# Kernel optimization log

Measured on AMD Instinct MI355X. Metric: run time of the kernel, lower is better.

Reference implementation:

```python
import jax, jax.numpy as jnp
import numpy as np

DIM = 768
H = 12
HEAD = DIM // H
SCALE = HEAD ** -0.5
NMM, NV, NA = 8, 4, 4


def _cross_attn(x1, x2, qw, kvw, pw, pb):
    # x1: [B,N1,C] queries, x2: [B,N2,C] keys/values. Weights stored [in,out].
    B, N1, C = x1.shape
    N2 = x2.shape[1]
    q = (x1 @ qw).reshape(B, N1, H, HEAD).transpose(0, 2, 1, 3)        # [B,H,N1,d]
    kv = (x2 @ kvw).reshape(B, N2, 2, H, HEAD)
    k = kv[:, :, 0].transpose(0, 2, 1, 3)                               # [B,H,N2,d]
    v = kv[:, :, 1].transpose(0, 2, 1, 3)
    attn = jax.nn.softmax(jnp.einsum('bhnd,bhmd->bhnm', q, k) * SCALE, axis=-1)
    o = jnp.einsum('bhnm,bhmd->bhnd', attn, v).transpose(0, 2, 1, 3).reshape(B, N1, C)
    return o @ pw + pb, attn


def setup_inputs() -> dict:
    key = jax.random.key(0)
    ks = jax.random.split(key, 16)
    s = 0.02
    inp = {
        'xmm': jax.random.normal(ks[0], (64, 16, DIM), jnp.float32),
        'xv': jax.random.normal(ks[1], (64, 784, DIM), jnp.float32),
        'xa': jax.random.normal(ks[2], (64, 512, DIM), jnp.float32),
        # visual cross-attn params (weights stored [in,out] = torch W.T)
        'qv_w': s * jax.random.normal(ks[3], (DIM, DIM), jnp.float32),
        'kvv_w': s * jax.random.normal(ks[4], (DIM, 2 * DIM), jnp.float32),
        'projv_w': s * jax.random.normal(ks[5], (DIM, DIM), jnp.float32),
        'projv_b': jnp.zeros((DIM,), jnp.float32),
        # audio cross-attn params
        'qa_w': s * jax.random.normal(ks[6], (DIM, DIM), jnp.float32),
        'kva_w': s * jax.random.normal(ks[7], (DIM, 2 * DIM), jnp.float32),
        'proja_w': s * jax.random.normal(ks[8], (DIM, DIM), jnp.float32),
        'proja_b': jnp.zeros((DIM,), jnp.float32),
        # factorized fusion attention params (dim_ratio=1.0 -> inner dim = DIM)
        'fq_w': s * jax.random.normal(ks[9], (DIM, DIM), jnp.float32),
        'fk_w': s * jax.random.normal(ks[10], (2 * DIM, DIM), jnp.float32),
        'fv_w': s * jax.random.normal(ks[11], (2 * DIM, DIM), jnp.float32),
        'fproj_w': s * jax.random.normal(ks[12], (DIM, DIM), jnp.float32),
        'fproj_b': jnp.zeros((DIM,), jnp.float32),
    }
    return inp


def reference(xmm, xv, xa, qv_w, kvv_w, projv_w, projv_b,
              qa_w, kva_w, proja_w, proja_b,
              fq_w, fk_w, fv_w, fproj_w, fproj_b):
    B = xmm.shape[0]
    xmm2 = xmm[:, :NMM]
    xmm_v, _ = _cross_attn(xmm[:, NMM:NMM + NV], xv, qv_w, kvv_w, projv_w, projv_b)
    xmm_a, _ = _cross_attn(xmm[:, NMM + NV:], xa, qa_w, kva_w, proja_w, proja_b)
    # outer-product token fusion: [B, NV*NA, 2*DIM]
    xva = jnp.concatenate([
        jnp.broadcast_to(xmm_v[:, :, None, :], (B, NV, NA, DIM)),
        jnp.broadcast_to(xmm_a[:, None, :, :], (B, NV, NA, DIM)),
    ], axis=-1).reshape(B, NV * NA, 2 * DIM)
    q = (xmm2 @ fq_w).reshape(B, NMM, H, -1).transpose(0, 2, 1, 3)
    k = (xva @ fk_w).reshape(B, NV * NA, H, -1).transpose(0, 2, 1, 3)
    v = (xva @ fv_w).reshape(B, NV * NA, H, -1).transpose(0, 2, 1, 3)
    attn = jax.nn.softmax(jnp.einsum('bhnd,bhmd->bhnm', q, k) * SCALE, axis=-1)
    o = jnp.einsum('bhnm,bhmd->bhnd', attn, v).transpose(0, 2, 1, 3).reshape(B, NMM, DIM)
    o = o @ fproj_w + fproj_b
    xmm_out = jnp.concatenate([o, xmm_v, xmm_a], axis=1)  # [B,16,DIM]
    return xmm_out, attn
```

## Files before the change

### kernel.cpp

```cpp
#include <hip/hip_runtime.h>
#include <stdint.h>

typedef unsigned short u16;
typedef unsigned int u32;
typedef __attribute__((ext_vector_type(8))) short short8;
typedef __attribute__((ext_vector_type(4))) float floatx4;


__device__ __forceinline__ u16 f2bf_rne(float f) {
  u32 u = __float_as_uint(f);
  return (u16)((u + 0x7fffu + ((u >> 16) & 1u)) >> 16);
}
__device__ __forceinline__ u32 pack_rne_u(u32 a, u32 b) {
  a += 0x7fffu + ((a >> 16) & 1u);
  b += 0x7fffu + ((b >> 16) & 1u);
  return __builtin_amdgcn_perm(b, a, 0x07060302u);
}

__device__ __forceinline__ void block_sync_lds() {
  asm volatile("s_waitcnt lgkmcnt(0)" ::: "memory");
  __builtin_amdgcn_s_barrier();
  asm volatile("" ::: "memory");
}

__device__ __forceinline__ void sg_body(
    float (*sAt)[20], float (*sW)[64],
    const float* __restrict__ A, int a_pitch, int a_rb, int a_off,
    const float* __restrict__ W, const float* __restrict__ bias,
    float* __restrict__ Cout, int c_pitch, int c_rb, int c_off,
    int rt, int n0)
{
  const int t = threadIdx.x;
  const int g = t >> 6;
  const int c = t & 63;

  float acc[4] = {0.f, 0.f, 0.f, 0.f};

  for (int ks = 0; ks < 12; ++ks) {
    {
      int r = t >> 4;
      int c4 = (t & 15) * 4;
      int lr = rt * 16 + r;
      int grow = (lr / a_rb) * a_pitch + a_off + (lr % a_rb);
      float4 v = *(const float4*)(A + (size_t)grow * 768 + ks * 64 + c4);
      sAt[c4 + 0][r] = v.x;
      sAt[c4 + 1][r] = v.y;
      sAt[c4 + 2][r] = v.z;
      sAt[c4 + 3][r] = v.w;
    }
#pragma unroll
    for (int u = 0; u < 4; ++u) {
      int unit = t + u * 256;
      int r = unit >> 4;
      int c4 = (unit & 15) * 4;
      *(float4*)&sW[r][c4] = *(const float4*)(W + (size_t)(ks * 64 + r) * 768 + n0 + c4);
    }
    __syncthreads();
#pragma unroll 8
    for (int k = 0; k < 64; ++k) {
      float4 a4 = *(const float4*)&sAt[k][g * 4];
      float w = sW[k][c];
      acc[0] += a4.x * w;
      acc[1] += a4.y * w;
      acc[2] += a4.z * w;
      acc[3] += a4.w * w;
    }
    __syncthreads();
  }

  float bs = bias ? bias[n0 + c] : 0.f;
#pragma unroll
  for (int rr = 0; rr < 4; ++rr) {
    int lr = rt * 16 + g * 4 + rr;
    int grow = (lr / c_rb) * c_pitch + c_off + (lr % c_rb);
    Cout[(size_t)grow * 768 + n0 + c] = acc[rr] + bs;
  }
}

__global__ __launch_bounds__(256) void qproj(
    const float* __restrict__ xmm,
    const float* __restrict__ qv_w, const float* __restrict__ qa_w,
    const float* __restrict__ fq_w,
    float* __restrict__ q_v, float* __restrict__ q_a, float* __restrict__ q_f)
{
  __shared__ float sAt[64][20];
  __shared__ float sW[64][64];
  int rt = blockIdx.x;
  int n0 = blockIdx.y * 64;
  if (rt < 16)
    sg_body(sAt, sW, xmm, 16, 4, 8, qv_w, nullptr, q_v, 4, 4, 0, rt, n0);
  else if (rt < 32)
    sg_body(sAt, sW, xmm, 16, 4, 12, qa_w, nullptr, q_a, 4, 4, 0, rt - 16, n0);
  else
    sg_body(sAt, sW, xmm, 16, 8, 0, fq_w, nullptr, q_f, 8, 8, 0, rt - 32, n0);
}

__global__ __launch_bounds__(256) void proj2(
    const float* __restrict__ o_v, const float* __restrict__ o_a,
    const float* __restrict__ projv_w, const float* __restrict__ projv_b,
    const float* __restrict__ proja_w, const float* __restrict__ proja_b,
    float* __restrict__ out0)
{
  __shared__ float sAt[64][20];
  __shared__ float sW[64][64];
  int z = blockIdx.z;
  sg_body(sAt, sW, z ? o_a : o_v, 4, 4, 0,
          z ? proja_w : projv_w, z ? proja_b : projv_b,
          out0, 16, 4, z ? 12 : 8, blockIdx.x, blockIdx.y * 64);
}

__global__ __launch_bounds__(256) void fkv(
    const float* __restrict__ out0,
    const float* __restrict__ fk_w, const float* __restrict__ fv_w,
    float* __restrict__ kbase)
{
  __shared__ float sAt[64][20];
  __shared__ float sW[64][64];
  int z = blockIdx.z;
  const float* W = (z < 2) ? (fk_w + (size_t)(z & 1) * 768 * 768)
                           : (fv_w + (size_t)(z & 1) * 768 * 768);
  int a_off = (z & 1) ? 12 : 8;
  sg_body(sAt, sW, out0, 16, 4, a_off, W, nullptr,
          kbase + (size_t)z * 256 * 768, 4, 4, 0, blockIdx.x, blockIdx.y * 64);
}

__global__ __launch_bounds__(256) void fproj(
    const float* __restrict__ o_f,
    const float* __restrict__ fproj_w, const float* __restrict__ fproj_b,
    float* __restrict__ out0)
{
  __shared__ float sAt[64][20];
  __shared__ float sW[64][64];
  sg_body(sAt, sW, o_f, 8, 8, 0, fproj_w, fproj_b, out0, 16, 8, 0,
          blockIdx.x, blockIdx.y * 64);
}

__global__ __launch_bounds__(256) void qtilde(
    const float* __restrict__ q_v, const float* __restrict__ q_a,
    const float* __restrict__ kvv_w, const float* __restrict__ kva_w,
    u16* __restrict__ Qt_v, u16* __restrict__ Qt_a)
{
  __shared__ float sAt[64][20];
  __shared__ float sW[64][65];

  const int rt = blockIdx.x;
  const int nt = blockIdx.y;
  const int path = blockIdx.z / 12;
  const int h = blockIdx.z % 12;
  const float* q = path ? q_a : q_v;
  const float* kvw = path ? kva_w : kvv_w;
  u16* Qt = path ? Qt_a : Qt_v;

  const int t = threadIdx.x;
  const int g = t >> 6;
  const int c = t & 63;
  const int n0 = nt * 64;

  {
    int r = t >> 4;
    int c4 = (t & 15) * 4;
    float4 v = *(const float4*)(q + (size_t)(rt * 16 + r) * 768 + h * 64 + c4);
    sAt[c4 + 0][r] = v.x;
    sAt[c4 + 1][r] = v.y;
    sAt[c4 + 2][r] = v.z;
    sAt[c4 + 3][r] = v.w;
  }
#pragma unroll
  for (int u = 0; u < 4; ++u) {
    int unit = t + u * 256;
    int d = unit >> 4;
    int c4 = (unit & 15) * 4;
    float4 v = *(const float4*)(kvw + (size_t)(n0 + d) * 1536 + h * 64 + c4);
    sW[d][c4 + 0] = v.x;
    sW[d][c4 + 1] = v.y;
    sW[d][c4 + 2] = v.z;
    sW[d][c4 + 3] = v.w;
  }
  __syncthreads();

  float acc[4] = {0.f, 0.f, 0.f, 0.f};
#pragma unroll 16
  for (int e = 0; e < 64; ++e) {
    float4 a4 = *(const float4*)&sAt[e][g * 4];
    float w = sW[c][e];
    acc[0] += a4.x * w;
    acc[1] += a4.y * w;
    acc[2] += a4.z * w;
    acc[3] += a4.w * w;
  }
#pragma unroll
  for (int rr = 0; rr < 4; ++rr) {
    int rl = rt * 16 + g * 4 + rr;
    Qt[((size_t)(rl >> 2) * 48 + h * 4 + (rl & 3)) * 768 + n0 + c] = f2bf_rne(acc[rr]);
  }
}

__global__ __launch_bounds__(256) void attn_logits(
    const u16* __restrict__ Qt_v, const u16* __restrict__ Qt_a,
    const float* __restrict__ Xv, const float* __restrict__ Xa,
    float* __restrict__ Sv, float* __restrict__ Sa)
{
  const int z = blockIdx.z;
  const int jt = blockIdx.x;
  if (z == 1 && jt >= 4) return;
  const u16* Qt = z ? Qt_a : Qt_v;
  const float* X = z ? Xa : Xv;
  float* S = z ? Sa : Sv;
  const int N2 = z ? 512 : 784;

  __shared__ __align__(16) u16 sX[2][128 * 64];

  const int t = threadIdx.x;
  const int lane = t & 63;
  const int wave = t >> 6;
  const int b = blockIdx.y;
  const int j0 = jt * 128;
  const int jmax = (N2 - j0 < 128) ? (N2 - j0) : 128;
  const u16* Qb = Qt + (size_t)b * 48 * 768;
  const float* Xb = X + (size_t)b * N2 * 768;

  const int xr_r = t >> 3;
  const int xc = (t & 7) * 8;
  const int qrow0 = lane & 15;
  const int qcb = (lane >> 4) * 8;

  floatx4 acc[3][2];
#pragma unroll
  for (int i = 0; i < 3; ++i)
#pragma unroll
    for (int j = 0; j < 2; ++j) acc[i][j] = (floatx4){0.f, 0.f, 0.f, 0.f};

  uint4 xA[4][2], xB[4][2];
  short8 qr[3][2];

#define AL_LOADX(dst, ks_)                                                     \
  do {                                                                         \
    _Pragma("unroll") for (int u = 0; u < 4; ++u) {                            \
      int r_ = xr_r + u * 32;                                                  \
      uint4 a0_ = {0u, 0u, 0u, 0u}, a1_ = {0u, 0u, 0u, 0u};                    \
      if (r_ < jmax) {                                                         \
        const uint4* s_ =                                                      \
            (const uint4*)(Xb + (size_t)(j0 + r_) * 768 + (ks_) * 64 + xc);    \
        a0_ = s_[0];                                                           \
        a1_ = s_[1];                                                           \
      }                                                                        \
      dst[u][0] = a0_;                                                         \
      dst[u][1] = a1_;                                                         \
    }                                                                          \
  } while (0)

#define AL_LOADQ(ks_)                                                          \
  do {                                                                         \
    _Pragma("unroll") for (int i = 0; i < 3; ++i)                              \
      _Pragma("unroll") for (int kk = 0; kk < 2; ++kk)                         \
        qr[i][kk] = *(const short8*)(Qb + (size_t)(i * 16 + qrow0) * 768 +     \
                                     (ks_) * 64 + kk * 32 + qcb);              \
  } while (0)

#define AL_WRITEX(src, bufp)                                                   \
  do {                                                                         \
    _Pragma("unroll") for (int u = 0; u < 4; ++u) {                            \
      int r_ = xr_r + u * 32;                                                  \
      uint4 pk_;                                                               \
      pk_.x = pack_rne_u(src[u][0].x, src[u][0].y);                            \
      pk_.y = pack_rne_u(src[u][0].z, src[u][0].w);                            \
      pk_.z = pack_rne_u(src[u][1].x, src[u][1].y);                            \
      pk_.w = pack_rne_u(src[u][1].z, src[u][1].w);                            \
      *(uint4*)((bufp) + r_ * 64 + (xc ^ ((r_ & 7) * 8))) = pk_;               \
    }                                                                          \
  } while (0)

#define AL_COMPUTE(bufp)                                                       \
  do {                                                                         \
    _Pragma("unroll") for (int kk = 0; kk < 2; ++kk) {                         \
      short8 bfr_[2];                                                          \
      _Pragma("unroll") for (int jj = 0; jj < 2; ++jj) {                       \
        int jr_ = wave * 32 + jj * 16 + qrow0;                                 \
        int kb_ = kk * 32 + qcb;                                               \
        bfr_[jj] =                                                             \
            *(const short8*)((bufp) + jr_ * 64 + (kb_ ^ ((jr_ & 7) * 8)));     \
      }                                                                        \
      _Pragma("unroll") for (int i = 0; i < 3; ++i)                            \
        _Pragma("unroll") for (int jj = 0; jj < 2; ++jj)                       \
          acc[i][jj] = __builtin_amdgcn_mfma_f32_16x16x32_bf16(                \
              qr[i][kk], bfr_[jj], acc[i][jj], 0, 0, 0);                       \
    }                                                                          \
  } while (0)

  u16* sX0 = &sX[0][0];
  u16* sX1 = &sX[1][0];

  AL_LOADX(xA, 0);
  AL_LOADQ(0);
#pragma unroll
  for (int ks = 0; ks < 12; ks += 2) {
    AL_LOADX(xB, ks + 1);
    AL_WRITEX(xA, sX0);
    block_sync_lds();
    AL_COMPUTE(sX0);
    AL_LOADQ(ks + 1);
    if (ks + 2 < 12) AL_LOADX(xA, ks + 2);
    AL_WRITEX(xB, sX1);
    block_sync_lds();
    AL_COMPUTE(sX1);
    if (ks + 2 < 12) AL_LOADQ(ks + 2);
  }
#undef AL_LOADX
#undef AL_LOADQ
#undef AL_WRITEX
#undef AL_COMPUTE

  const int quad = lane >> 4;
  const int lc = lane & 15;
#pragma unroll
  for (int i = 0; i < 3; ++i)
#pragma unroll
    for (int jj = 0; jj < 2; ++jj) {
      int col = j0 + wave * 32 + jj * 16 + lc;
      if (col < N2) {
        int row0 = i * 16 + quad * 4;
#pragma unroll
        for (int r = 0; r < 4; ++r)
          S[((size_t)b * 48 + row0 + r) * N2 + col] = acc[i][jj][r] * 0.125f;
      }
    }
}

__global__ __launch_bounds__(256) void softmax_p(
    const float* __restrict__ Sv, const float* __restrict__ Sa,
    u16* __restrict__ Pv, u16* __restrict__ Pa)
{
  const int z = blockIdx.z;
  const float* S = z ? Sa : Sv;
  u16* P = z ? Pa : Pv;
  const int N2 = z ? 512 : 784;
  const int N2p = z ? 512 : 832;

  const int hh = blockIdx.x;
  const int b = blockIdx.y;
  const int t = threadIdx.x;
  const int lane = t & 63;
  const int wave = t >> 6;
  const int row = hh * 4 + wave;
  const float* Srow = S + ((size_t)b * 48 + row) * N2;
  u16* Prow = P + ((size_t)b * 48 + row) * N2p;

  float m = -1e30f;
  for (int j = lane; j < N2; j += 64) m = fmaxf(m, Srow[j]);
#pragma unroll
  for (int off = 32; off > 0; off >>= 1) m = fmaxf(m, __shfl_xor(m, off));

  float e[13];
  float l = 0.f;
  int cnt = 0;
  for (int j = lane; j < N2; j += 64) {
    float p = __expf(Srow[j] - m);
    e[cnt++] = p;
    l += p;
  }
#pragma unroll
  for (int off = 32; off > 0; off >>= 1) l += __shfl_xor(l, off);
  float inv = 1.0f / l;

  cnt = 0;
  for (int j = lane; j < N2; j += 64) Prow[j] = f2bf_rne(e[cnt++] * inv);
  for (int j = N2 + lane; j < N2p; j += 64) Prow[j] = 0;
}

__global__ __launch_bounds__(256) void attn_px(
    const u16* __restrict__ Pv, const u16* __restrict__ Pa,
    const float* __restrict__ Xv, const float* __restrict__ Xa,
    float* __restrict__ Ov, float* __restrict__ Oa)
{
  const int z = blockIdx.z;
  const u16* P = z ? Pa : Pv;
  const float* X = z ? Xa : Xv;
  float* O = z ? Oa : Ov;
  const int N2 = z ? 512 : 784;
  const int N2p = z ? 512 : 832;

  __shared__ __align__(16) u16 sXT[2][128 * 72];

  const int t = threadIdx.x;
  const int lane = t & 63;
  const int wave = t >> 6;
  const int nt = blockIdx.x;
  const int b = blockIdx.y;
  const int n0 = nt * 128;
  const u16* Pb = P + (size_t)b * 48 * N2p;
  const float* Xb = X + (size_t)b * N2 * 768;
  const int Ks = N2p >> 6;

  const int jp0 = t >> 5;
  const int nq4 = (t & 31) * 4;
  const int qrow0 = lane & 15;
  const int qcb = (lane >> 4) * 8;

  floatx4 acc[3][2];
#pragma unroll
  for (int i = 0; i < 3; ++i)
#pragma unroll
    for (int j = 0; j < 2; ++j) acc[i][j] = (floatx4){0.f, 0.f, 0.f, 0.f};

  uint4 xA[4][2], xB[4][2];
  short8 qr[3][2];

#define PX_LOADX(dst, ks_)                                                     \
  do {                                                                         \
    _Pragma("unroll") for (int u = 0; u < 4; ++u) {                            \
      int j_ = (ks_) * 64 + (jp0 + u * 8) * 2;                                 \
      uint4 a0_ = {0u, 0u, 0u, 0u}, a1_ = {0u, 0u, 0u, 0u};                    \
      if (j_ < N2)                                                             \
        a0_ = *(const uint4*)(Xb + (size_t)j_ * 768 + n0 + nq4);               \
      if (j_ + 1 < N2)                                                         \
        a1_ = *(const uint4*)(Xb + (size_t)(j_ + 1) * 768 + n0 + nq4);         \
      dst[u][0] = a0_;                                                         \
      dst[u][1] = a1_;                                                         \
    }                                                                          \
  } while (0)

#define PX_LOADP(ks_)                                                          \
  do {                                                                         \
    _Pragma("unroll") for (int i = 0; i < 3; ++i)                              \
      _Pragma("unroll") for (int kk = 0; kk < 2; ++kk)                         \
        qr[i][kk] = *(const short8*)(Pb + (size_t)(i * 16 + qrow0) * N2p +     \
                                     (ks_) * 64 + kk * 32 + qcb);              \
  } while (0)

#define PX_WRITEX(src, bufp)                                                   \
  do {                                                                         \
    _Pragma("unroll") for (int u = 0; u < 4; ++u) {                            \
      int jl_ = (jp0 + u * 8) * 2;                                             \
      u32 w0_ = pack_rne_u(src[u][0].x, src[u][1].x);                          \
      u32 w1_ = pack_rne_u(src[u][0].y, src[u][1].y);                          \
      u32 w2_ = pack_rne_u(src[u][0].z, src[u][1].z);                          \
      u32 w3_ = pack_rne_u(src[u][0].w, src[u][1].w);                          \
      _Pragma("unroll") for (int m_ = 0; m_ < 4; ++m_) {                       \
        int n_ = nq4 + m_;                                                     \
        int sw_ = (((n_ >> 2) & 7) ^ ((n_ & 3) << 1)) * 8;                     \
        u32 wv_ = (m_ == 0) ? w0_ : (m_ == 1) ? w1_ : (m_ == 2) ? w2_ : w3_;   \
        *(u32*)((bufp) + n_ * 72 + (jl_ ^ sw_)) = wv_;                         \
      }                                                                        \
    }                                                                          \
  } while (0)

#define PX_COMPUTE(bufp)                                                       \
  do {                                                                         \
    _Pragma("unroll") for (int kk = 0; kk < 2; ++kk) {                         \
      _Pragma("unroll") for (int jj = 0; jj < 2; ++jj) {                       \
        int n_ = wave * 32 + jj * 16 + qrow0;                                  \
        int sw_ = (((n_ >> 2) & 7) ^ ((n_ & 3) << 1)) * 8;                     \
        int kb_ = kk * 32 + qcb;                                               \
        short8 bfr_ = *(const short8*)((bufp) + n_ * 72 + (kb_ ^ sw_));        \
        _Pragma("unroll") for (int i = 0; i < 3; ++i)                          \
          acc[i][jj] = __builtin_amdgcn_mfma_f32_16x16x32_bf16(                \
              qr[i][kk], bfr_, acc[i][jj], 0, 0, 0);                           \
      }                                                                        \
    }                                                                          \
  } while (0)

  u16* sT0 = &sXT[0][0];
  u16* sT1 = &sXT[1][0];

  PX_LOADX(xA, 0);
  PX_LOADP(0);
  int ks = 0;
  for (;;) {
    int more0 = (ks + 1 < Ks);
    if (more0) PX_LOADX(xB, ks + 1);
    PX_WRITEX(xA, sT0);
    block_sync_lds();
    PX_COMPUTE(sT0);
    if (!more0) break;
    PX_LOADP(ks + 1);
    ++ks;
    int more1 = (ks + 1 < Ks);
    if (more1) PX_LOADX(xA, ks + 1);
    PX_WRITEX(xB, sT1);
    block_sync_lds();
    PX_COMPUTE(sT1);
    if (!more1) break;
    PX_LOADP(ks + 1);
    ++ks;
  }
#undef PX_LOADX
#undef PX_LOADP
#undef PX_WRITEX
#undef PX_COMPUTE

  const int quad = lane >> 4;
  const int lc = lane & 15;
#pragma unroll
  for (int i = 0; i < 3; ++i)
#pragma unroll
    for (int jj = 0; jj < 2; ++jj) {
      int col = n0 + wave * 32 + jj * 16 + lc;
      int row0 = i * 16 + quad * 4;
#pragma unroll
      for (int r = 0; r < 4; ++r)
        O[((size_t)b * 48 + row0 + r) * 768 + col] = acc[i][jj][r];
    }
}

__global__ __launch_bounds__(256) void omix(
    const float* __restrict__ O_v, const float* __restrict__ O_a,
    const float* __restrict__ kvv_w, const float* __restrict__ kva_w,
    float* __restrict__ o_v, float* __restrict__ o_a)
{
  __shared__ float sAt[64][20];
  __shared__ float sW[64][64];

  const int z = blockIdx.z;
  const float* Ob = z ? O_a : O_v;
  const float* kvw = z ? kva_w : kvv_w;
  float* oo = z ? o_a : o_v;

  const int rt = blockIdx.x;
  const int h = blockIdx.y;
  const int t = threadIdx.x;
  const int g = t >> 6;
  const int c = t & 63;

  float acc[4] = {0.f, 0.f, 0.f, 0.f};

  for (int ks = 0; ks < 12; ++ks) {
    {
      int r = t >> 4;
      int c4 = (t & 15) * 4;
      int rl = rt * 16 + r;
      int arow = (rl >> 2) * 48 + h * 4 + (rl & 3);
      float4 v = *(const float4*)(Ob + (size_t)arow * 768 + ks * 64 + c4);
      sAt[c4 + 0][r] = v.x;
      sAt[c4 + 1][r] = v.y;
      sAt[c4 + 2][r] = v.z;
      sAt[c4 + 3][r] = v.w;
    }
#pragma unroll
    for (int u = 0; u < 4; ++u) {
      int unit = t + u * 256;
      int k = unit >> 4;
      int c4 = (unit & 15) * 4;
      *(float4*)&sW[k][c4] = *(const float4*)(kvw + (size_t)(ks * 64 + k) * 1536 + 768 + h * 64 + c4);
    }
    __syncthreads();
#pragma unroll 8
    for (int k = 0; k < 64; ++k) {
      float4 a4 = *(const float4*)&sAt[k][g * 4];
      float w = sW[k][c];
      acc[0] += a4.x * w;
      acc[1] += a4.y * w;
      acc[2] += a4.z * w;
      acc[3] += a4.w * w;
    }
    __syncthreads();
  }

#pragma unroll
  for (int rr = 0; rr < 4; ++rr) {
    int rl = rt * 16 + g * 4 + rr;
    oo[(size_t)rl * 768 + h * 64 + c] = acc[rr];
  }
}

__global__ __launch_bounds__(256) void fusion_attn(
    const float* __restrict__ Qf,
    const float* __restrict__ K1, const float* __restrict__ K2,
    const float* __restrict__ V1, const float* __restrict__ V2,
    float* __restrict__ Of,
    float* __restrict__ AttnOut)
{
  const int h = blockIdx.x;
  const int b = blockIdx.y;
  const int t = threadIdx.x;
  const int lane = t & 63;
  const int wave = t >> 6;

  __shared__ float sQ[8][64];
  __shared__ float sK1[4][64], sK2[4][64], sV1[4][64], sV2[4][64];
  __shared__ float sP[8][16];

  for (int idx = t; idx < 512; idx += 256)
    sQ[idx >> 6][idx & 63] = Qf[((size_t)(b * 8 + (idx >> 6))) * 768 + h * 64 + (idx & 63)];
  {
    size_t base = ((size_t)(b * 4 + wave)) * 768 + h * 64 + lane;
    sK1[wave][lane] = K1[base];
    sK2[wave][lane] = K2[base];
    sV1[wave][lane] = V1[base];
    sV2[wave][lane] = V2[base];
  }
  __syncthreads();

  if (t < 128) {
    int qi = t >> 4, m = t & 15, iv = m >> 2, ja = m & 3;
    float s = 0.f;
#pragma unroll
    for (int d = 0; d < 64; ++d) s += sQ[qi][d] * (sK1[iv][d] + sK2[ja][d]);
    s *= 0.125f;
    float mx = s;
#pragma unroll
    for (int off = 8; off > 0; off >>= 1) mx = fmaxf(mx, __shfl_xor(mx, off, 16));
    float p = __expf(s - mx);
    float l = p;
#pragma unroll
    for (int off = 8; off > 0; off >>= 1) l += __shfl_xor(l, off, 16);
    p = p / l;
    sP[qi][m] = p;
    AttnOut[(((size_t)b * 12 + h) * 8 + qi) * 16 + m] = p;
  }
  __syncthreads();

  for (int idx = t; idx < 512; idx += 256) {
    int qi = idx >> 6, d = idx & 63;
    float o = 0.f;
#pragma unroll
    for (int m = 0; m < 16; ++m) o += sP[qi][m] * (sV1[m >> 2][d] + sV2[m & 3][d]);
    Of[((size_t)(b * 8 + qi)) * 768 + h * 64 + d] = o;
  }
}

extern "C" void kernel_launch(void* const* d_in, const int* in_sizes, int n_in,
                              void* d_out, int out_size, void* d_ws, size_t ws_size,
                              hipStream_t stream)
{
  const float* xmm     = (const float*)d_in[0];
  const float* xv      = (const float*)d_in[1];
  const float* xa      = (const float*)d_in[2];
  const float* qv_w    = (const float*)d_in[3];
  const float* kvv_w   = (const float*)d_in[4];
  const float* projv_w = (const float*)d_in[5];
  const float* projv_b = (const float*)d_in[6];
  const float* qa_w    = (const float*)d_in[7];
  const float* kva_w   = (const float*)d_in[8];
  const float* proja_w = (const float*)d_in[9];
  const float* proja_b = (const float*)d_in[10];
  const float* fq_w    = (const float*)d_in[11];
  const float* fk_w    = (const float*)d_in[12];
  const float* fv_w    = (const float*)d_in[13];
  const float* fproj_w = (const float*)d_in[14];
  const float* fproj_b = (const float*)d_in[15];

  float* out0 = (float*)d_out;
  float* out1 = out0 + (size_t)64 * 16 * 768;

  char* ws = (char*)d_ws;
  size_t off = 0;
  float* q_v  = (float*)(ws + off); off += (size_t)256 * 768 * 4;
  float* q_a  = (float*)(ws + off); off += (size_t)256 * 768 * 4;
  float* q_f  = (float*)(ws + off); off += (size_t)512 * 768 * 4;
  u16*   Qt_v = (u16*)(ws + off);   off += (size_t)64 * 48 * 768 * 2;
  u16*   Qt_a = (u16*)(ws + off);   off += (size_t)64 * 48 * 768 * 2;
  float* S_v  = (float*)(ws + off); off += (size_t)64 * 48 * 784 * 4;
  float* S_a  = (float*)(ws + off); off += (size_t)64 * 48 * 512 * 4;
  u16*   P_v  = (u16*)(ws + off);   off += (size_t)64 * 48 * 832 * 2;
  u16*   P_a  = (u16*)(ws + off);   off += (size_t)64 * 48 * 512 * 2;
  float* O_v  = (float*)(ws + off); off += (size_t)64 * 48 * 768 * 4;
  float* O_a  = (float*)(ws + off); off += (size_t)64 * 48 * 768 * 4;
  float* o_v  = (float*)(ws + off); off += (size_t)256 * 768 * 4;
  float* o_a  = (float*)(ws + off); off += (size_t)256 * 768 * 4;
  float* kbase = (float*)(ws + off); off += (size_t)4 * 256 * 768 * 4;
  float* o_f  = (float*)(ws + off); off += (size_t)512 * 768 * 4;

  float* k1 = kbase;
  float* k2 = kbase + (size_t)256 * 768;
  float* v1 = kbase + (size_t)2 * 256 * 768;
  float* v2 = kbase + (size_t)3 * 256 * 768;

  qproj<<<dim3(64, 12), 256, 0, stream>>>(xmm, qv_w, qa_w, fq_w, q_v, q_a, q_f);
  qtilde<<<dim3(16, 12, 24), 256, 0, stream>>>(q_v, q_a, kvv_w, kva_w, Qt_v, Qt_a);
  attn_logits<<<dim3(7, 64, 2), 256, 0, stream>>>(Qt_v, Qt_a, xv, xa, S_v, S_a);
  softmax_p<<<dim3(12, 64, 2), 256, 0, stream>>>(S_v, S_a, P_v, P_a);
  attn_px<<<dim3(6, 64, 2), 256, 0, stream>>>(P_v, P_a, xv, xa, O_v, O_a);
  omix<<<dim3(16, 12, 2), 256, 0, stream>>>(O_v, O_a, kvv_w, kva_w, o_v, o_a);
  proj2<<<dim3(16, 12, 2), 256, 0, stream>>>(o_v, o_a, projv_w, projv_b, proja_w, proja_b, out0);
  fkv<<<dim3(16, 12, 4), 256, 0, stream>>>(out0, fk_w, fv_w, kbase);
  fusion_attn<<<dim3(12, 64), 256, 0, stream>>>(q_f, k1, k2, v1, v2, o_f, out1);
  fproj<<<dim3(32, 12), 256, 0, stream>>>(o_f, fproj_w, fproj_b, out0);
}
```

Measured before the change: 589.1 us.

## Restructure attn_logits into single-wave 16-row tiles with full-K LDS staging

Result: slower. 618.2 us (+4.9%).

```diff
diff --git a/kernel.cpp b/kernel.cpp
--- a/kernel.cpp
+++ b/kernel.cpp
@@ -15,6 +15,11 @@
   a += 0x7fffu + ((a >> 16) & 1u);
   b += 0x7fffu + ((b >> 16) & 1u);
   return __builtin_amdgcn_perm(b, a, 0x07060302u);
+}
+__device__ __forceinline__ void gld_lds16(const void* g, void* l) {
+  __builtin_amdgcn_global_load_lds(
+      (__attribute__((address_space(1))) void*)(uintptr_t)g,
+      (__attribute__((address_space(3))) void*)l, 16, 0, 0);
 }
 
 __device__ __forceinline__ void block_sync_lds() {
@@ -195,135 +200,85 @@
   }
 }
 
-__global__ __launch_bounds__(256) void attn_logits(
+__global__ __launch_bounds__(64) void attn_logits(
     const u16* __restrict__ Qt_v, const u16* __restrict__ Qt_a,
     const float* __restrict__ Xv, const float* __restrict__ Xa,
     float* __restrict__ Sv, float* __restrict__ Sa)
 {
-  const int z = blockIdx.z;
-  const int jt = blockIdx.x;
-  if (z == 1 && jt >= 4) return;
-  const u16* Qt = z ? Qt_a : Qt_v;
-  const float* X = z ? Xa : Xv;
-  float* S = z ? Sa : Sv;
-  const int N2 = z ? 512 : 784;
-
-  __shared__ __align__(16) u16 sX[2][128 * 64];
-
-  const int t = threadIdx.x;
-  const int lane = t & 63;
-  const int wave = t >> 6;
+  const int bx = blockIdx.x;
   const int b = blockIdx.y;
-  const int j0 = jt * 128;
-  const int jmax = (N2 - j0 < 128) ? (N2 - j0) : 128;
+  const int isA = (bx >= 49);
+  const int T = isA ? (bx - 49) : bx;
+  const u16* Qt = isA ? Qt_a : Qt_v;
+  const float* X = isA ? Xa : Xv;
+  float* S = isA ? Sa : Sv;
+  const int N2 = isA ? 512 : 784;
+
+  __shared__ __align__(16) u16 sX[16 * 768];
+
+  const int lane = threadIdx.x;
+  const int j0 = T * 16;
+  const u32* Xt = (const u32*)(X + ((size_t)b * N2 + j0) * 768);
   const u16* Qb = Qt + (size_t)b * 48 * 768;
-  const float* Xb = X + (size_t)b * N2 * 768;
-
-  const int xr_r = t >> 3;
-  const int xc = (t & 7) * 8;
-  const int qrow0 = lane & 15;
-  const int qcb = (lane >> 4) * 8;
-
-  floatx4 acc[3][2];
-#pragma unroll
-  for (int i = 0; i < 3; ++i)
-#pragma unroll
-    for (int j = 0; j < 2; ++j) acc[i][j] = (floatx4){0.f, 0.f, 0.f, 0.f};
-
-  uint4 xA[4][2], xB[4][2];
-  short8 qr[3][2];
-
-#define AL_LOADX(dst, ks_)                                                     \
+  const int ql = lane & 15;
+  const int qs = lane >> 4;
+
+  uint4 ra[6], rb[6];
+
+#define L3_LOAD(buf, c_)                                                       \
   do {                                                                         \
-    _Pragma("unroll") for (int u = 0; u < 4; ++u) {                            \
-      int r_ = xr_r + u * 32;                                                  \
-      uint4 a0_ = {0u, 0u, 0u, 0u}, a1_ = {0u, 0u, 0u, 0u};                    \
-      if (r_ < jmax) {                                                         \
-        const uint4* s_ =                                                      \
-            (const uint4*)(Xb + (size_t)(j0 + r_) * 768 + (ks_) * 64 + xc);    \
-        a0_ = s_[0];                                                           \
-        a1_ = s_[1];                                                           \
-      }                                                                        \
-      dst[u][0] = a0_;                                                         \
-      dst[u][1] = a1_;                                                         \
+    _Pragma("unroll") for (int i = 0; i < 6; ++i)                              \
+      buf[i] = *(const uint4*)(Xt + (c_) * 1536 + i * 256 + lane * 4);         \
+  } while (0)
+
+#define L3_PACK(buf, c_)                                                       \
+  do {                                                                         \
+    _Pragma("unroll") for (int i = 0; i < 6; ++i) {                            \
+      int jr_ = (c_) * 2 + i / 3;                                              \
+      int colb_ = (i % 3) * 512 + lane * 8;                                    \
+      uint2 w_;                                                                \
+      w_.x = pack_rne_u(buf[i].x, buf[i].y);                                   \
+      w_.y = pack_rne_u(buf[i].z, buf[i].w);                                   \
+      *(uint2*)((char*)sX + jr_ * 1536 + (colb_ ^ ((jr_ & 7) << 4))) = w_;     \
     }                                                                          \
   } while (0)
 
-#define AL_LOADQ(ks_)                                                          \
-  do {                                                                         \
-    _Pragma("unroll") for (int i = 0; i < 3; ++i)                              \
-      _Pragma("unroll") for (int kk = 0; kk < 2; ++kk)                         \
-        qr[i][kk] = *(const short8*)(Qb + (size_t)(i * 16 + qrow0) * 768 +     \
-                                     (ks_) * 64 + kk * 32 + qcb);              \
-  } while (0)
-
-#define AL_WRITEX(src, bufp)                                                   \
-  do {                                                                         \
-    _Pragma("unroll") for (int u = 0; u < 4; ++u) {                            \
-      int r_ = xr_r + u * 32;                                                  \
-      uint4 pk_;                                                               \
-      pk_.x = pack_rne_u(src[u][0].x, src[u][0].y);                            \
-      pk_.y = pack_rne_u(src[u][0].z, src[u][0].w);                            \
-      pk_.z = pack_rne_u(src[u][1].x, src[u][1].y);                            \
-      pk_.w = pack_rne_u(src[u][1].z, src[u][1].w);                            \
-      *(uint4*)((bufp) + r_ * 64 + (xc ^ ((r_ & 7) * 8))) = pk_;               \
-    }                                                                          \
-  } while (0)
-
-#define AL_COMPUTE(bufp)                                                       \
-  do {                                                                         \
-    _Pragma("unroll") for (int kk = 0; kk < 2; ++kk) {                         \
-      short8 bfr_[2];                                                          \
-      _Pragma("unroll") for (int jj = 0; jj < 2; ++jj) {                       \
-        int jr_ = wave * 32 + jj * 16 + qrow0;                                 \
-        int kb_ = kk * 32 + qcb;                                               \
-        bfr_[jj] =                                                             \
-            *(const short8*)((bufp) + jr_ * 64 + (kb_ ^ ((jr_ & 7) * 8)));     \
-      }                                                                        \
-      _Pragma("unroll") for (int i = 0; i < 3; ++i)                            \
-        _Pragma("unroll") for (int jj = 0; jj < 2; ++jj)                       \
-          acc[i][jj] = __builtin_amdgcn_mfma_f32_16x16x32_bf16(                \
-              qr[i][kk], bfr_[jj], acc[i][jj], 0, 0, 0);                       \
-    }                                                                          \
-  } while (0)
-
-  u16* sX0 = &sX[0][0];
-  u16* sX1 = &sX[1][0];
-
-  AL_LOADX(xA, 0);
-  AL_LOADQ(0);
-#pragma unroll
-  for (int ks = 0; ks < 12; ks += 2) {
-    AL_LOADX(xB, ks + 1);
-    AL_WRITEX(xA, sX0);
-    block_sync_lds();
-    AL_COMPUTE(sX0);
-    AL_LOADQ(ks + 1);
-    if (ks + 2 < 12) AL_LOADX(xA, ks + 2);
-    AL_WRITEX(xB, sX1);
-    block_sync_lds();
-    AL_COMPUTE(sX1);
-    if (ks + 2 < 12) AL_LOADQ(ks + 2);
-  }
-#undef AL_LOADX
-#undef AL_LOADQ
-#undef AL_WRITEX
-#undef AL_COMPUTE
-
-  const int quad = lane >> 4;
-  const int lc = lane & 15;
+  L3_LOAD(ra, 0);
+#pragma unroll
+  for (int c = 0; c < 8; ++c) {
+    if (c + 1 < 8) {
+      if (c & 1) L3_LOAD(ra, c + 1);
+      else       L3_LOAD(rb, c + 1);
+    }
+    if (c & 1) L3_PACK(rb, c);
+    else       L3_PACK(ra, c);
+  }
+#undef L3_LOAD
+#undef L3_PACK
+  asm volatile("s_waitcnt lgkmcnt(0)" ::: "memory");
+
+  floatx4 acc[3];
+#pragma unroll
+  for (int i = 0; i < 3; ++i) acc[i] = (floatx4){0.f, 0.f, 0.f, 0.f};
+
+#pragma unroll 4
+  for (int kk = 0; kk < 24; ++kk) {
+    short8 bf = *(const short8*)((char*)sX + ql * 1536 +
+                                 ((kk * 64 + qs * 16) ^ ((ql & 7) << 4)));
+#pragma unroll
+    for (int i = 0; i < 3; ++i) {
+      short8 qa = *(const short8*)(Qb + (size_t)(i * 16 + ql) * 768 +
+                                   kk * 32 + qs * 8);
+      acc[i] = __builtin_amdgcn_mfma_f32_16x16x32_bf16(qa, bf, acc[i], 0, 0, 0);
+    }
+  }
+
 #pragma unroll
   for (int i = 0; i < 3; ++i)
 #pragma unroll
-    for (int jj = 0; jj < 2; ++jj) {
-      int col = j0 + wave * 32 + jj * 16 + lc;
-      if (col < N2) {
-        int row0 = i * 16 + quad * 4;
-#pragma unroll
-        for (int r = 0; r < 4; ++r)
-          S[((size_t)b * 48 + row0 + r) * N2 + col] = acc[i][jj][r] * 0.125f;
-      }
-    }
+    for (int r = 0; r < 4; ++r)
+      S[((size_t)b * 48 + i * 16 + qs * 4 + r) * N2 + j0 + ql] =
+          acc[i][r] * 0.125f;
 }
 
 __global__ __launch_bounds__(256) void softmax_p(
@@ -667,7 +622,7 @@
 
   qproj<<<dim3(64, 12), 256, 0, stream>>>(xmm, qv_w, qa_w, fq_w, q_v, q_a, q_f);
   qtilde<<<dim3(16, 12, 24), 256, 0, stream>>>(q_v, q_a, kvv_w, kva_w, Qt_v, Qt_a);
-  attn_logits<<<dim3(7, 64, 2), 256, 0, stream>>>(Qt_v, Qt_a, xv, xa, S_v, S_a);
+  attn_logits<<<dim3(81, 64), 64, 0, stream>>>(Qt_v, Qt_a, xv, xa, S_v, S_a);
   softmax_p<<<dim3(12, 64, 2), 256, 0, stream>>>(S_v, S_a, P_v, P_a);
   attn_px<<<dim3(6, 64, 2), 256, 0, stream>>>(P_v, P_a, xv, xa, O_v, O_a);
   omix<<<dim3(16, 12, 2), 256, 0, stream>>>(O_v, O_a, kvv_w, kva_w, o_v, o_a);
```
